# Kernel tuning notes

Hardware: AMD Instinct MI355X
Metric: run time of the kernel (lower is better)

Reference implementation:

```python
import jax, jax.numpy as jnp
import numpy as np

DIM = 512
NUM_HEADS = 8
HEAD_DIM = DIM // NUM_HEADS
SCALE = HEAD_DIM ** -0.5


def setup_inputs() -> dict:
    key = jax.random.key(0)
    k1, k2, k3, k4 = jax.random.split(key, 4)
    x = jax.random.normal(k1, (4, 2048, DIM), dtype=jnp.float32)
    W_qkv = jax.random.normal(k2, (DIM, 3 * DIM), dtype=jnp.float32) * (DIM ** -0.5)
    W_proj = jax.random.normal(k3, (DIM, DIM), dtype=jnp.float32) * (DIM ** -0.5)
    b_proj = jax.random.normal(k4, (DIM,), dtype=jnp.float32) * 0.01
    return {"x": x, "W_qkv": W_qkv, "W_proj": W_proj, "b_proj": b_proj}


def reference(x, W_qkv, W_proj, b_proj):
    B, N, C = x.shape
    H, hd = NUM_HEADS, HEAD_DIM
    # qkv: [B, N, 3, H, hd] -> (q, k, v) each [B, H, N, hd]
    qkv = (x @ W_qkv).reshape(B, N, 3, H, hd)
    qkv = jnp.transpose(qkv, (2, 0, 3, 1, 4))
    q, k, v = qkv[0], qkv[1], qkv[2]
    # eager attention: [B, H, N, N]
    attn = jnp.einsum('bhnd,bhmd->bhnm', q, k) * SCALE
    attn = jax.nn.softmax(attn, axis=-1)
    out = jnp.einsum('bhnm,bhmd->bhnd', attn, v)  # [B, H, N, hd]
    out = jnp.transpose(out, (0, 2, 1, 3)).reshape(B, N, C)
    out = out @ W_proj + b_proj
    return (out, k, v)
```

## Files before the change

kernel.cpp:

```cpp
#include <hip/hip_runtime.h>

typedef unsigned short ushort_t;
typedef __bf16 bf16x8 __attribute__((ext_vector_type(8)));
typedef __bf16 bf16x4 __attribute__((ext_vector_type(4)));
typedef ushort_t u16x8 __attribute__((ext_vector_type(8)));
typedef float f32x4 __attribute__((ext_vector_type(4)));

#define MFMA(a, b, c) __builtin_amdgcn_mfma_f32_16x16x32_bf16(a, b, c, 0, 0, 0)

#if __has_builtin(__builtin_amdgcn_mfma_f32_16x16x16bf16_1k)
typedef short s16x4 __attribute__((ext_vector_type(4)));
__device__ __forceinline__ f32x4 mfma16(bf16x4 a, bf16x4 b, f32x4 c) {
    union { bf16x4 v; s16x4 s; } ua, ub; ua.v = a; ub.v = b;
    return __builtin_amdgcn_mfma_f32_16x16x16bf16_1k(ua.s, ub.s, c, 0, 0, 0);
}
#define MFMA16_ASM 0
#elif __has_builtin(__builtin_amdgcn_mfma_f32_16x16x16_bf16)
__device__ __forceinline__ f32x4 mfma16(bf16x4 a, bf16x4 b, f32x4 c) {
    return __builtin_amdgcn_mfma_f32_16x16x16_bf16(a, b, c, 0, 0, 0);
}
#define MFMA16_ASM 0
#else
__device__ __forceinline__ f32x4 mfma16(bf16x4 a, bf16x4 b, f32x4 c) {
    asm("v_mfma_f32_16x16x16_bf16 %0, %1, %2, %0" : "+v"(c) : "v"(a), "v"(b));
    return c;
}
#define MFMA16_ASM 1
#endif

#define N_X      4194304L
#define N_WQKV   786432L
#define N_WPROJ  262144L
#define OUT_OFF_K 4194304L
#define OUT_OFF_V 8388608L

#define OFF_FLAG   0UL
#define OFF_XB     1024UL
#define OFF_WQKVT  (OFF_XB + 8388608UL)
#define OFF_WPROJT (OFF_WQKVT + 1572864UL)
#define OFF_BPROJ  (OFF_WPROJT + 524288UL)
#define OFF_QB     (OFF_BPROJ + 2048UL)
#define OFF_KB     (OFF_QB + 8388608UL)
#define OFF_VTB    (OFF_KB + 8388608UL)
#define OFF_ATTN   (OFF_VTB + 8388608UL)

#define QSCALE 0.180336880519191f

__device__ __forceinline__ ushort_t f2b(float f) {
    union { float f; unsigned u; } v; v.f = f;
    return (ushort_t)((v.u + 0x7FFFu + ((v.u >> 16) & 1u)) >> 16);
}
__device__ __forceinline__ ushort_t f2b_trunc(float f) {
    union { float f; unsigned u; } v; v.f = f;
    return (ushort_t)(v.u >> 16);
}
__device__ __forceinline__ float b2f(ushort_t h) {
    union { unsigned u; float f; } v; v.u = ((unsigned)h) << 16;
    return v.f;
}

__device__ __forceinline__ float fast_exp2(float x) {
#if __has_builtin(__builtin_amdgcn_exp2f)
    return __builtin_amdgcn_exp2f(x);
#else
    return __expf(x * 0.6931471805599453f);
#endif
}

__device__ __forceinline__ void glds16(const void* g, const void* l) {
    __builtin_amdgcn_global_load_lds((__attribute__((address_space(1))) void*)g,
                                     (__attribute__((address_space(3))) void*)l,
                                     16, 0, 0);
}

__device__ __forceinline__ int detect_bf16(const unsigned* __restrict__ x) {
    int lane = threadIdx.x & 63;
    int cnt = 0;
#pragma unroll
    for (int i = 0; i < 4; ++i) {
        unsigned w = x[lane + i * 64];
        float v = __uint_as_float((w & 0xFFFFu) << 16);
        float a = fabsf(v);
        if (a > 1e-3f && a < 100.0f) cnt++;
    }
#pragma unroll
    for (int off = 1; off < 64; off <<= 1) cnt += __shfl_xor(cnt, off, 64);
    return cnt > 128;
}

__global__ void k_prep(const void* __restrict__ xv, const void* __restrict__ wqv,
                       const void* __restrict__ wpv, const void* __restrict__ bpv,
                       ushort_t* __restrict__ xb, ushort_t* __restrict__ wqT,
                       ushort_t* __restrict__ wpT, float* __restrict__ bpf) {
    const int isb = detect_bf16((const unsigned*)xv);
    long i0 = (long)blockIdx.x * blockDim.x + threadIdx.x;
    long stride = (long)gridDim.x * blockDim.x;
    if (isb) {
        const ushort_t* x = (const ushort_t*)xv;
        const ushort_t* wq = (const ushort_t*)wqv;
        const ushort_t* wp = (const ushort_t*)wpv;
        const ushort_t* bp = (const ushort_t*)bpv;
        for (long i = i0; i < N_X / 8; i += stride)
            ((u16x8*)xb)[i] = ((const u16x8*)x)[i];
        for (long i = i0; i < N_WQKV / 8; i += stride) {
            long n = (i * 8) >> 9, k = (i * 8) & 511;
            u16x8 o;
#pragma unroll
            for (int e = 0; e < 8; ++e) o[e] = wq[(k + e) * 1536 + n];
            ((u16x8*)wqT)[i] = o;
        }
        for (long i = i0; i < N_WPROJ / 8; i += stride) {
            long n = (i * 8) >> 9, k = (i * 8) & 511;
            u16x8 o;
#pragma unroll
            for (int e = 0; e < 8; ++e) o[e] = wp[(k + e) * 512 + n];
            ((u16x8*)wpT)[i] = o;
        }
        for (long i = i0; i < 512; i += stride) bpf[i] = b2f(bp[i]);
    } else {
        const float* x = (const float*)xv;
        const float* wq = (const float*)wqv;
        const float* wp = (const float*)wpv;
        const float* bp = (const float*)bpv;
        for (long i = i0; i < N_X / 8; i += stride) {
            f32x4 a = ((const f32x4*)x)[i * 2], b = ((const f32x4*)x)[i * 2 + 1];
            u16x8 o;
#pragma unroll
            for (int e = 0; e < 4; ++e) { o[e] = f2b(a[e]); o[e + 4] = f2b(b[e]); }
            ((u16x8*)xb)[i] = o;
        }
        for (long i = i0; i < N_WQKV / 8; i += stride) {
            long n = (i * 8) >> 9, k = (i * 8) & 511;
            u16x8 o;
#pragma unroll
            for (int e = 0; e < 8; ++e) o[e] = f2b(wq[(k + e) * 1536 + n]);
            ((u16x8*)wqT)[i] = o;
        }
        for (long i = i0; i < N_WPROJ / 8; i += stride) {
            long n = (i * 8) >> 9, k = (i * 8) & 511;
            u16x8 o;
#pragma unroll
            for (int e = 0; e < 8; ++e) o[e] = f2b(wp[(k + e) * 512 + n]);
            ((u16x8*)wpT)[i] = o;
        }
        for (long i = i0; i < 512; i += stride) bpf[i] = bp[i];
    }
}

__global__ __launch_bounds__(256, 2)
void k_qkv(const unsigned* __restrict__ xraw,
           const ushort_t* __restrict__ xb, const ushort_t* __restrict__ wqT,
           ushort_t* __restrict__ qb, ushort_t* __restrict__ kb, ushort_t* __restrict__ vb,
           void* __restrict__ dout) {
    const int isb = detect_bf16(xraw);
    __shared__ __align__(16) ushort_t As[2][128 * 32];
    __shared__ __align__(16) ushort_t Bs[2][128 * 32];
    const int tid = threadIdx.x, wave = tid >> 6, lane = tid & 63;
    const int id = blockIdx.x;
    const int xcd = id & 7, g = id >> 3;
    const int bx = xcd * 8 + (g & 7);
    const int by = g >> 3;
    const int tm = bx * 128, tn = by * 128;
    const int wm = (wave >> 1) * 64, wn = (wave & 1) * 64;
    const int l15 = lane & 15, lq = lane >> 4;
    const int srow = lane >> 2, sc = lane & 3;

    f32x4 acc[4][4];
#pragma unroll
    for (int a = 0; a < 4; ++a)
#pragma unroll
        for (int b = 0; b < 4; ++b) acc[a][b] = (f32x4){0.f, 0.f, 0.f, 0.f};

    auto stage = [&](int k0, int buf) {
#pragma unroll
        for (int t = 0; t < 2; ++t) {
            int s = wave * 2 + t;
            int row = s * 16 + srow;
            int c = (sc ^ (row >> 1)) & 3;
            glds16(xb  + (long)(tm + row) * 512 + k0 + c * 8, &As[buf][s * 512]);
            glds16(wqT + (long)(tn + row) * 512 + k0 + c * 8, &Bs[buf][s * 512]);
        }
    };

    stage(0, 0);
    for (int ks = 0; ks < 16; ++ks) {
        int cur = ks & 1;
        if (ks < 15) {
            stage((ks + 1) * 32, cur ^ 1);
            asm volatile("s_waitcnt vmcnt(4)" ::: "memory");
        } else {
            asm volatile("s_waitcnt vmcnt(0)" ::: "memory");
        }
        __builtin_amdgcn_sched_barrier(0);
        __builtin_amdgcn_s_barrier();

        const ushort_t* Ac = &As[cur][0];
        const ushort_t* Bc = &Bs[cur][0];
        bf16x8 af[4], bfr[4];
#pragma unroll
        for (int mt = 0; mt < 4; ++mt) {
            int row = wm + mt * 16 + l15;
            int cp = (lq ^ (row >> 1)) & 3;
            af[mt] = *(const bf16x8*)(Ac + row * 32 + cp * 8);
        }
#pragma unroll
        for (int nt = 0; nt < 4; ++nt) {
            int row = wn + nt * 16 + l15;
            int cp = (lq ^ (row >> 1)) & 3;
            bfr[nt] = *(const bf16x8*)(Bc + row * 32 + cp * 8);
        }
#pragma unroll
        for (int mt = 0; mt < 4; ++mt)
#pragma unroll
            for (int nt = 0; nt < 4; ++nt)
                acc[mt][nt] = MFMA(af[mt], bfr[nt], acc[mt][nt]);

        asm volatile("s_waitcnt lgkmcnt(0)" ::: "memory");
        __builtin_amdgcn_sched_barrier(0);
        __builtin_amdgcn_s_barrier();
    }

    float*    koutf = (float*)dout + OUT_OFF_K;
    float*    voutf = (float*)dout + OUT_OFF_V;
    ushort_t* koutb = (ushort_t*)dout + OUT_OFF_K;
    ushort_t* voutb = (ushort_t*)dout + OUT_OFF_V;
#pragma unroll
    for (int mt = 0; mt < 4; ++mt) {
#pragma unroll
        for (int nt = 0; nt < 4; ++nt) {
            int j = tn + wn + nt * 16 + l15;
            int t = j >> 9, h = (j >> 6) & 7, d = j & 63;
#pragma unroll
            for (int r = 0; r < 4; ++r) {
                int mm = tm + wm + mt * 16 + lq * 4 + r;
                int b = mm >> 11, nn = mm & 2047;
                float v = acc[mt][nt][r];
                long idx = ((long)(b * 8 + h) * 2048 + nn) * 64 + d;
                if (t == 0) {
                    qb[idx] = f2b(v * QSCALE);
                } else if (t == 1) {
                    kb[idx] = f2b(v);
                    if (isb) koutb[idx] = f2b(v); else koutf[idx] = v;
                } else {
                    vb[idx] = f2b(v);
                    if (isb) voutb[idx] = f2b(v); else voutf[idx] = v;
                }
            }
        }
    }
}

__global__ __launch_bounds__(256, 4)
void k_vtrans(const ushort_t* __restrict__ vb, ushort_t* __restrict__ vtb) {
    __shared__ ushort_t T[64 * 64];
    const int tid = threadIdx.x;
    const int bh = blockIdx.y, ktile = blockIdx.x;
    const long base = (long)bh * 131072 + (long)ktile * 64 * 64;
    const int row = tid >> 2, cq = tid & 3;
#pragma unroll
    for (int half = 0; half < 2; ++half) {
        int c = cq + half * 4;
        u16x8 v = *(const u16x8*)(vb + base + row * 64 + c * 8);
#pragma unroll
        for (int e = 0; e < 8; ++e) {
            int dim = c * 8 + e;
            T[row * 64 + ((dim + row) & 63)] = v[e];
        }
    }
    __syncthreads();
#pragma unroll
    for (int it = 0; it < 16; ++it) {
        int d = (tid >> 6) * 16 + it;
        int key = tid & 63;
        vtb[(long)bh * 131072 + (long)d * 2048 + ktile * 64 + key] =
            T[key * 64 + ((d + key) & 63)];
    }
}

__global__ __launch_bounds__(256, 2)
void k_attn(const ushort_t* __restrict__ qb, const ushort_t* __restrict__ kb,
            const ushort_t* __restrict__ vtb, ushort_t* __restrict__ attnb) {
    __shared__ __align__(16) ushort_t Kt[2][128 * 64];
    __shared__ __align__(16) ushort_t Vt[2][64 * 128];
    const int tid = threadIdx.x, wave = tid >> 6, lane = tid & 63;
    const int l15 = lane & 15, lq = lane >> 4;
    const int id = blockIdx.x;
    const int xcd = id & 7, g = id >> 3;
    const int bh = xcd * 4 + (g >> 4);
    const int qt = g & 15;
    const long kvbase = (long)bh * 131072;
    const long qbase = kvbase + (long)qt * 128 * 64;

    const int ksrow = lane >> 3, kschunk = lane & 7;
    const int vsrow = lane >> 4, vschunk = lane & 15;

    auto stage = [&](int j, int buf) {
#pragma unroll
        for (int t = 0; t < 4; ++t) {
            int s = wave * 4 + t;
            {
                int row = s * 8 + ksrow;
                int c = kschunk ^ (row & 7);
                glds16(kb + kvbase + (long)(j * 128 + row) * 64 + c * 8, &Kt[buf][s * 512]);
            }
            {
                int row = s * 4 + vsrow;
                int c = vschunk ^ (row & 15);
                glds16(vtb + kvbase + (long)row * 2048 + j * 128 + c * 8, &Vt[buf][s * 512]);
            }
        }
    };

    stage(0, 0);

    bf16x8 aQ[2][2];
#pragma unroll
    for (int mq = 0; mq < 2; ++mq)
#pragma unroll
        for (int kt = 0; kt < 2; ++kt)
            aQ[mq][kt] = *(const bf16x8*)(qb + qbase +
                (long)(wave * 32 + mq * 16 + l15) * 64 + kt * 32 + lq * 8);

    f32x4 oacc[2][4];
#pragma unroll
    for (int mq = 0; mq < 2; ++mq)
#pragma unroll
        for (int nd = 0; nd < 4; ++nd) oacc[mq][nd] = (f32x4){0.f, 0.f, 0.f, 0.f};
    float ssum[2] = {0.f, 0.f};

    for (int j = 0; j < 16; ++j) {
        int cur = j & 1;
        if (j < 15) {
            stage(j + 1, cur ^ 1);
            asm volatile("s_waitcnt vmcnt(8)" ::: "memory");
        } else {
            asm volatile("s_waitcnt vmcnt(0)" ::: "memory");
        }
        __builtin_amdgcn_sched_barrier(0);
        __builtin_amdgcn_s_barrier();

        const ushort_t* Ktc = &Kt[cur][0];
        const ushort_t* Vtc = &Vt[cur][0];

#pragma unroll
        for (int h = 0; h < 2; ++h) {
            f32x4 sacc[2][4];
#pragma unroll
            for (int mq = 0; mq < 2; ++mq)
#pragma unroll
                for (int nt = 0; nt < 4; ++nt) sacc[mq][nt] = (f32x4){0.f, 0.f, 0.f, 0.f};
#pragma unroll
            for (int nt = 0; nt < 4; ++nt) {
                int krow = h * 64 + nt * 16 + l15;
#pragma unroll
                for (int kt = 0; kt < 2; ++kt) {
                    int c = (kt * 4 + lq) ^ (krow & 7);
                    bf16x8 bk = *(const bf16x8*)(Ktc + krow * 64 + c * 8);
                    sacc[0][nt] = MFMA(bk, aQ[0][kt], sacc[0][nt]);
                    sacc[1][nt] = MFMA(bk, aQ[1][kt], sacc[1][nt]);
                }
            }
            bf16x4 pb[2][4];
#pragma unroll
            for (int mq = 0; mq < 2; ++mq) {
#pragma unroll
                for (int nt = 0; nt < 4; ++nt) {
                    union { ushort_t u[4]; bf16x4 v; } pk;
                    float acc0 = 0.f, acc1 = 0.f;
#pragma unroll
                    for (int r = 0; r < 4; ++r) {
                        float p = fast_exp2(sacc[mq][nt][r]);
                        ushort_t tt = f2b_trunc(p);
                        pk.u[r] = tt;
                        if (r & 1) acc1 += b2f(tt); else acc0 += b2f(tt);
                    }
                    ssum[mq] += acc0 + acc1;
                    pb[mq][nt] = pk.v;
                }
            }
#pragma unroll
            for (int nd = 0; nd < 4; ++nd) {
                int drow = nd * 16 + l15;
#pragma unroll
                for (int nt = 0; nt < 4; ++nt) {
                    int kc = h * 8 + nt * 2 + (lq >> 1);
                    int cc = kc ^ (drow & 15);
                    bf16x4 va = *(const bf16x4*)(Vtc + drow * 128 + cc * 8 + (lq & 1) * 4);
                    oacc[0][nd] = mfma16(va, pb[0][nt], oacc[0][nd]);
                    oacc[1][nd] = mfma16(va, pb[1][nt], oacc[1][nd]);
                }
            }
        }

        asm volatile("s_waitcnt lgkmcnt(0)" ::: "memory");
        __builtin_amdgcn_sched_barrier(0);
        __builtin_amdgcn_s_barrier();
    }

#if MFMA16_ASM
    asm volatile("s_nop 7\n\ts_nop 7");
#endif
    const int b = bh >> 3, hh = bh & 7;
#pragma unroll
    for (int mq = 0; mq < 2; ++mq) {
        float s = ssum[mq];
        s += __shfl_xor(s, 16, 64);
        s += __shfl_xor(s, 32, 64);
        float inv = 1.0f / s;
        int n = qt * 128 + wave * 32 + mq * 16 + l15;
        long rowbase = ((long)b * 2048 + n) * 512 + hh * 64;
#pragma unroll
        for (int nd = 0; nd < 4; ++nd) {
            int d0 = nd * 16 + lq * 4;
            union { ushort_t u[4]; unsigned long long ll; } o;
#pragma unroll
            for (int r = 0; r < 4; ++r) o.u[r] = f2b(oacc[mq][nd][r] * inv);
            *(unsigned long long*)(attnb + rowbase + d0) = o.ll;
        }
    }
}

__global__ __launch_bounds__(256, 2)
void k_proj(const unsigned* __restrict__ xraw,
            const ushort_t* __restrict__ ab, const ushort_t* __restrict__ wpT,
            const float* __restrict__ bpf, void* __restrict__ dout) {
    const int isb = detect_bf16(xraw);
    __shared__ __align__(16) ushort_t As[2][128 * 32];
    __shared__ __align__(16) ushort_t Bs[2][128 * 32];
    const int tid = threadIdx.x, wave = tid >> 6, lane = tid & 63;
    const int id = blockIdx.x;
    const int xcd = id & 7, g = id >> 3;
    const int bx = xcd * 8 + (g & 7);
    const int by = g >> 3;
    const int tm = bx * 128, tn = by * 128;
    const int wm = (wave >> 1) * 64, wn = (wave & 1) * 64;
    const int l15 = lane & 15, lq = lane >> 4;
    const int srow = lane >> 2, sc = lane & 3;

    f32x4 acc[4][4];
#pragma unroll
    for (int a = 0; a < 4; ++a)
#pragma unroll
        for (int b = 0; b < 4; ++b) acc[a][b] = (f32x4){0.f, 0.f, 0.f, 0.f};

    auto stage = [&](int k0, int buf) {
#pragma unroll
        for (int t = 0; t < 2; ++t) {
            int s = wave * 2 + t;
            int row = s * 16 + srow;
            int c = (sc ^ (row >> 1)) & 3;
            glds16(ab  + (long)(tm + row) * 512 + k0 + c * 8, &As[buf][s * 512]);
            glds16(wpT + (long)(tn + row) * 512 + k0 + c * 8, &Bs[buf][s * 512]);
        }
    };

    stage(0, 0);
    for (int ks = 0; ks < 16; ++ks) {
        int cur = ks & 1;
        if (ks < 15) {
            stage((ks + 1) * 32, cur ^ 1);
            asm volatile("s_waitcnt vmcnt(4)" ::: "memory");
        } else {
            asm volatile("s_waitcnt vmcnt(0)" ::: "memory");
        }
        __builtin_amdgcn_sched_barrier(0);
        __builtin_amdgcn_s_barrier();

        const ushort_t* Ac = &As[cur][0];
        const ushort_t* Bc = &Bs[cur][0];
        bf16x8 af[4], bfr[4];
#pragma unroll
        for (int mt = 0; mt < 4; ++mt) {
            int row = wm + mt * 16 + l15;
            int cp = (lq ^ (row >> 1)) & 3;
            af[mt] = *(const bf16x8*)(Ac + row * 32 + cp * 8);
        }
#pragma unroll
        for (int nt = 0; nt < 4; ++nt) {
            int row = wn + nt * 16 + l15;
            int cp = (lq ^ (row >> 1)) & 3;
            bfr[nt] = *(const bf16x8*)(Bc + row * 32 + cp * 8);
        }
#pragma unroll
        for (int mt = 0; mt < 4; ++mt)
#pragma unroll
            for (int nt = 0; nt < 4; ++nt)
                acc[mt][nt] = MFMA(af[mt], bfr[nt], acc[mt][nt]);

        asm volatile("s_waitcnt lgkmcnt(0)" ::: "memory");
        __builtin_amdgcn_sched_barrier(0);
        __builtin_amdgcn_s_barrier();
    }

#pragma unroll
    for (int mt = 0; mt < 4; ++mt) {
#pragma unroll
        for (int nt = 0; nt < 4; ++nt) {
            int j = tn + wn + nt * 16 + l15;
            float bias = bpf[j];
#pragma unroll
            for (int r = 0; r < 4; ++r) {
                int mm = tm + wm + mt * 16 + lq * 4 + r;
                float v = acc[mt][nt][r] + bias;
                if (isb) ((ushort_t*)dout)[(long)mm * 512 + j] = f2b(v);
                else     ((float*)dout)[(long)mm * 512 + j] = v;
            }
        }
    }
}

extern "C" void kernel_launch(void* const* d_in, const int* in_sizes, int n_in,
                              void* d_out, int out_size, void* d_ws, size_t ws_size,
                              hipStream_t stream) {
    (void)in_sizes; (void)n_in; (void)out_size; (void)ws_size;
    char* ws = (char*)d_ws;
    ushort_t* xb  = (ushort_t*)(ws + OFF_XB);
    ushort_t* wqT = (ushort_t*)(ws + OFF_WQKVT);
    ushort_t* wpT = (ushort_t*)(ws + OFF_WPROJT);
    float*    bpf = (float*)(ws + OFF_BPROJ);
    ushort_t* qb  = (ushort_t*)(ws + OFF_QB);
    ushort_t* kb  = (ushort_t*)(ws + OFF_KB);
    ushort_t* vtb = (ushort_t*)(ws + OFF_VTB);
    ushort_t* ab  = (ushort_t*)(ws + OFF_ATTN);
    ushort_t* vb  = (ushort_t*)(ws + OFF_ATTN);

    k_prep<<<1024, 256, 0, stream>>>(d_in[0], d_in[1], d_in[2], d_in[3],
                                     xb, wqT, wpT, bpf);

    k_qkv<<<768, 256, 0, stream>>>((const unsigned*)d_in[0], xb, wqT,
                                   qb, kb, vb, d_out);

    k_vtrans<<<dim3(32, 32), 256, 0, stream>>>(vb, vtb);

    k_attn<<<512, 256, 0, stream>>>(qb, kb, vtb, ab);

    k_proj<<<256, 256, 0, stream>>>((const unsigned*)d_in[0], ab, wpT, bpf, d_out);
}
```

Baseline: 180.5 us.

## Use 16x16x32 MFMA for PV with MFMA row sums; single-buffer GEMMs

The attention kernel now computes all 128 keys of a tile at once and permutes K rows at staging, so the exponentiated scores pack directly into bf16x8 operands. This lets the P·V product use the wider 16x16x32 MFMA instead of 16x16x16. Row sums are now produced by an MFMA against a ones vector, replacing the scalar accumulation and cross-lane shuffles, and P is converted with a rounding cast instead of truncation. Separately, the QKV and projection GEMMs drop their LDS double-buffered pipeline for a single buffer with __syncthreads, which gives up load/compute overlap in exchange for less LDS and simpler code.

```diff
diff --git a/kernel.cpp b/kernel.cpp
--- a/kernel.cpp
+++ b/kernel.cpp
@@ -2,31 +2,10 @@
 
 typedef unsigned short ushort_t;
 typedef __bf16 bf16x8 __attribute__((ext_vector_type(8)));
-typedef __bf16 bf16x4 __attribute__((ext_vector_type(4)));
 typedef ushort_t u16x8 __attribute__((ext_vector_type(8)));
 typedef float f32x4 __attribute__((ext_vector_type(4)));
 
 #define MFMA(a, b, c) __builtin_amdgcn_mfma_f32_16x16x32_bf16(a, b, c, 0, 0, 0)
-
-#if __has_builtin(__builtin_amdgcn_mfma_f32_16x16x16bf16_1k)
-typedef short s16x4 __attribute__((ext_vector_type(4)));
-__device__ __forceinline__ f32x4 mfma16(bf16x4 a, bf16x4 b, f32x4 c) {
-    union { bf16x4 v; s16x4 s; } ua, ub; ua.v = a; ub.v = b;
-    return __builtin_amdgcn_mfma_f32_16x16x16bf16_1k(ua.s, ub.s, c, 0, 0, 0);
-}
-#define MFMA16_ASM 0
-#elif __has_builtin(__builtin_amdgcn_mfma_f32_16x16x16_bf16)
-__device__ __forceinline__ f32x4 mfma16(bf16x4 a, bf16x4 b, f32x4 c) {
-    return __builtin_amdgcn_mfma_f32_16x16x16_bf16(a, b, c, 0, 0, 0);
-}
-#define MFMA16_ASM 0
-#else
-__device__ __forceinline__ f32x4 mfma16(bf16x4 a, bf16x4 b, f32x4 c) {
-    asm("v_mfma_f32_16x16x16_bf16 %0, %1, %2, %0" : "+v"(c) : "v"(a), "v"(b));
-    return c;
-}
-#define MFMA16_ASM 1
-#endif
 
 #define N_X      4194304L
 #define N_WQKV   786432L
@@ -49,10 +28,6 @@
 __device__ __forceinline__ ushort_t f2b(float f) {
     union { float f; unsigned u; } v; v.f = f;
     return (ushort_t)((v.u + 0x7FFFu + ((v.u >> 16) & 1u)) >> 16);
-}
-__device__ __forceinline__ ushort_t f2b_trunc(float f) {
-    union { float f; unsigned u; } v; v.f = f;
-    return (ushort_t)(v.u >> 16);
 }
 __device__ __forceinline__ float b2f(ushort_t h) {
     union { unsigned u; float f; } v; v.u = ((unsigned)h) << 16;
@@ -153,8 +128,8 @@
            ushort_t* __restrict__ qb, ushort_t* __restrict__ kb, ushort_t* __restrict__ vb,
            void* __restrict__ dout) {
     const int isb = detect_bf16(xraw);
-    __shared__ __align__(16) ushort_t As[2][128 * 32];
-    __shared__ __align__(16) ushort_t Bs[2][128 * 32];
+    __shared__ __align__(16) ushort_t As[128 * 32];
+    __shared__ __align__(16) ushort_t Bs[128 * 32];
     const int tid = threadIdx.x, wave = tid >> 6, lane = tid & 63;
     const int id = blockIdx.x;
     const int xcd = id & 7, g = id >> 3;
@@ -171,53 +146,35 @@
 #pragma unroll
         for (int b = 0; b < 4; ++b) acc[a][b] = (f32x4){0.f, 0.f, 0.f, 0.f};
 
-    auto stage = [&](int k0, int buf) {
+    for (int k0 = 0; k0 < 512; k0 += 32) {
 #pragma unroll
         for (int t = 0; t < 2; ++t) {
             int s = wave * 2 + t;
             int row = s * 16 + srow;
             int c = (sc ^ (row >> 1)) & 3;
-            glds16(xb  + (long)(tm + row) * 512 + k0 + c * 8, &As[buf][s * 512]);
-            glds16(wqT + (long)(tn + row) * 512 + k0 + c * 8, &Bs[buf][s * 512]);
-        }
-    };
-
-    stage(0, 0);
-    for (int ks = 0; ks < 16; ++ks) {
-        int cur = ks & 1;
-        if (ks < 15) {
-            stage((ks + 1) * 32, cur ^ 1);
-            asm volatile("s_waitcnt vmcnt(4)" ::: "memory");
-        } else {
-            asm volatile("s_waitcnt vmcnt(0)" ::: "memory");
-        }
-        __builtin_amdgcn_sched_barrier(0);
-        __builtin_amdgcn_s_barrier();
-
-        const ushort_t* Ac = &As[cur][0];
-        const ushort_t* Bc = &Bs[cur][0];
+            glds16(xb  + (long)(tm + row) * 512 + k0 + c * 8, As + s * 512);
+            glds16(wqT + (long)(tn + row) * 512 + k0 + c * 8, Bs + s * 512);
+        }
+        __syncthreads();
         bf16x8 af[4], bfr[4];
 #pragma unroll
         for (int mt = 0; mt < 4; ++mt) {
             int row = wm + mt * 16 + l15;
             int cp = (lq ^ (row >> 1)) & 3;
-            af[mt] = *(const bf16x8*)(Ac + row * 32 + cp * 8);
+            af[mt] = *(const bf16x8*)(As + row * 32 + cp * 8);
         }
 #pragma unroll
         for (int nt = 0; nt < 4; ++nt) {
             int row = wn + nt * 16 + l15;
             int cp = (lq ^ (row >> 1)) & 3;
-            bfr[nt] = *(const bf16x8*)(Bc + row * 32 + cp * 8);
+            bfr[nt] = *(const bf16x8*)(Bs + row * 32 + cp * 8);
         }
 #pragma unroll
         for (int mt = 0; mt < 4; ++mt)
 #pragma unroll
             for (int nt = 0; nt < 4; ++nt)
                 acc[mt][nt] = MFMA(af[mt], bfr[nt], acc[mt][nt]);
-
-        asm volatile("s_waitcnt lgkmcnt(0)" ::: "memory");
-        __builtin_amdgcn_sched_barrier(0);
-        __builtin_amdgcn_s_barrier();
+        __syncthreads();
     }
 
     float*    koutf = (float*)dout + OUT_OFF_K;
@@ -299,9 +256,11 @@
         for (int t = 0; t < 4; ++t) {
             int s = wave * 4 + t;
             {
-                int row = s * 8 + ksrow;
-                int c = kschunk ^ (row & 7);
-                glds16(kb + kvbase + (long)(j * 128 + row) * 64 + c * 8, &Kt[buf][s * 512]);
+                int p = s * 8 + ksrow;
+                int pos = p & 15;
+                int akey = ((p >> 5) << 5) + ((pos >> 2) << 3) + (pos & 3) + ((p >> 4) & 1) * 4;
+                int c = kschunk ^ (p & 7);
+                glds16(kb + kvbase + (long)(j * 128 + akey) * 64 + c * 8, &Kt[buf][s * 512]);
             }
             {
                 int row = s * 4 + vsrow;
@@ -321,12 +280,18 @@
             aQ[mq][kt] = *(const bf16x8*)(qb + qbase +
                 (long)(wave * 32 + mq * 16 + l15) * 64 + kt * 32 + lq * 8);
 
-    f32x4 oacc[2][4];
-#pragma unroll
-    for (int mq = 0; mq < 2; ++mq)
+    union { ushort_t u[8]; bf16x8 v; } oneu;
+#pragma unroll
+    for (int i = 0; i < 8; ++i) oneu.u[i] = 0x3F80;
+    const bf16x8 ones8 = oneu.v;
+
+    f32x4 oacc[2][4], sum_acc[2];
+#pragma unroll
+    for (int mq = 0; mq < 2; ++mq) {
 #pragma unroll
         for (int nd = 0; nd < 4; ++nd) oacc[mq][nd] = (f32x4){0.f, 0.f, 0.f, 0.f};
-    float ssum[2] = {0.f, 0.f};
+        sum_acc[mq] = (f32x4){0.f, 0.f, 0.f, 0.f};
+    }
 
     for (int j = 0; j < 16; ++j) {
         int cur = j & 1;
@@ -342,53 +307,44 @@
         const ushort_t* Ktc = &Kt[cur][0];
         const ushort_t* Vtc = &Vt[cur][0];
 
-#pragma unroll
-        for (int h = 0; h < 2; ++h) {
-            f32x4 sacc[2][4];
-#pragma unroll
-            for (int mq = 0; mq < 2; ++mq)
-#pragma unroll
-                for (int nt = 0; nt < 4; ++nt) sacc[mq][nt] = (f32x4){0.f, 0.f, 0.f, 0.f};
-#pragma unroll
-            for (int nt = 0; nt < 4; ++nt) {
-                int krow = h * 64 + nt * 16 + l15;
-#pragma unroll
-                for (int kt = 0; kt < 2; ++kt) {
-                    int c = (kt * 4 + lq) ^ (krow & 7);
-                    bf16x8 bk = *(const bf16x8*)(Ktc + krow * 64 + c * 8);
-                    sacc[0][nt] = MFMA(bk, aQ[0][kt], sacc[0][nt]);
-                    sacc[1][nt] = MFMA(bk, aQ[1][kt], sacc[1][nt]);
-                }
-            }
-            bf16x4 pb[2][4];
-#pragma unroll
-            for (int mq = 0; mq < 2; ++mq) {
-#pragma unroll
-                for (int nt = 0; nt < 4; ++nt) {
-                    union { ushort_t u[4]; bf16x4 v; } pk;
-                    float acc0 = 0.f, acc1 = 0.f;
-#pragma unroll
-                    for (int r = 0; r < 4; ++r) {
-                        float p = fast_exp2(sacc[mq][nt][r]);
-                        ushort_t tt = f2b_trunc(p);
-                        pk.u[r] = tt;
-                        if (r & 1) acc1 += b2f(tt); else acc0 += b2f(tt);
-                    }
-                    ssum[mq] += acc0 + acc1;
-                    pb[mq][nt] = pk.v;
-                }
-            }
+        f32x4 sacc[2][8];
+#pragma unroll
+        for (int mq = 0; mq < 2; ++mq)
+#pragma unroll
+            for (int nt = 0; nt < 8; ++nt) sacc[mq][nt] = (f32x4){0.f, 0.f, 0.f, 0.f};
+#pragma unroll
+        for (int nt = 0; nt < 8; ++nt) {
+            int krow = nt * 16 + l15;
+#pragma unroll
+            for (int kt = 0; kt < 2; ++kt) {
+                int c = (kt * 4 + lq) ^ (krow & 7);
+                bf16x8 bk = *(const bf16x8*)(Ktc + krow * 64 + c * 8);
+                sacc[0][nt] = MFMA(bk, aQ[0][kt], sacc[0][nt]);
+                sacc[1][nt] = MFMA(bk, aQ[1][kt], sacc[1][nt]);
+            }
+        }
+
+        bf16x8 pb8[2][4];
+#pragma unroll
+        for (int mq = 0; mq < 2; ++mq)
+#pragma unroll
+            for (int nt = 0; nt < 8; ++nt)
+#pragma unroll
+                for (int r = 0; r < 4; ++r)
+                    pb8[mq][nt >> 1][(nt & 1) * 4 + r] =
+                        (__bf16)fast_exp2(sacc[mq][nt][r]);
+
+#pragma unroll
+        for (int t = 0; t < 4; ++t) {
+            sum_acc[0] = MFMA(ones8, pb8[0][t], sum_acc[0]);
+            sum_acc[1] = MFMA(ones8, pb8[1][t], sum_acc[1]);
 #pragma unroll
             for (int nd = 0; nd < 4; ++nd) {
                 int drow = nd * 16 + l15;
-#pragma unroll
-                for (int nt = 0; nt < 4; ++nt) {
-                    int kc = h * 8 + nt * 2 + (lq >> 1);
-                    int cc = kc ^ (drow & 15);
-                    bf16x4 va = *(const bf16x4*)(Vtc + drow * 128 + cc * 8 + (lq & 1) * 4);
-                    oacc[0][nd] = mfma16(va, pb[0][nt], oacc[0][nd]);
-                    oacc[1][nd] = mfma16(va, pb[1][nt], oacc[1][nd]);
-                }
+                int cc = (t * 4 + lq) ^ (drow & 15);
+                bf16x8 va = *(const bf16x8*)(Vtc + drow * 128 + cc * 8);
+                oacc[0][nd] = MFMA(va, pb8[0][t], oacc[0][nd]);
+                oacc[1][nd] = MFMA(va, pb8[1][t], oacc[1][nd]);
             }
         }
 
@@ -397,16 +353,10 @@
         __builtin_amdgcn_s_barrier();
     }
 
-#if MFMA16_ASM
-    asm volatile("s_nop 7\n\ts_nop 7");
-#endif
     const int b = bh >> 3, hh = bh & 7;
 #pragma unroll
     for (int mq = 0; mq < 2; ++mq) {
-        float s = ssum[mq];
-        s += __shfl_xor(s, 16, 64);
-        s += __shfl_xor(s, 32, 64);
-        float inv = 1.0f / s;
+        float inv = 1.0f / sum_acc[mq][0];
         int n = qt * 128 + wave * 32 + mq * 16 + l15;
         long rowbase = ((long)b * 2048 + n) * 512 + hh * 64;
 #pragma unroll
@@ -425,8 +375,8 @@
             const ushort_t* __restrict__ ab, const ushort_t* __restrict__ wpT,
             const float* __restrict__ bpf, void* __restrict__ dout) {
     const int isb = detect_bf16(xraw);
-    __shared__ __align__(16) ushort_t As[2][128 * 32];
-    __shared__ __align__(16) ushort_t Bs[2][128 * 32];
+    __shared__ __align__(16) ushort_t As[128 * 32];
+    __shared__ __align__(16) ushort_t Bs[128 * 32];
     const int tid = threadIdx.x, wave = tid >> 6, lane = tid & 63;
     const int id = blockIdx.x;
     const int xcd = id & 7, g = id >> 3;
@@ -443,53 +393,35 @@
 #pragma unroll
         for (int b = 0; b < 4; ++b) acc[a][b] = (f32x4){0.f, 0.f, 0.f, 0.f};
 
-    auto stage = [&](int k0, int buf) {
+    for (int k0 = 0; k0 < 512; k0 += 32) {
 #pragma unroll
         for (int t = 0; t < 2; ++t) {
             int s = wave * 2 + t;
             int row = s * 16 + srow;
             int c = (sc ^ (row >> 1)) & 3;
-            glds16(ab  + (long)(tm + row) * 512 + k0 + c * 8, &As[buf][s * 512]);
-            glds16(wpT + (long)(tn + row) * 512 + k0 + c * 8, &Bs[buf][s * 512]);
-        }
-    };
-
-    stage(0, 0);
-    for (int ks = 0; ks < 16; ++ks) {
-        int cur = ks & 1;
-        if (ks < 15) {
-            stage((ks + 1) * 32, cur ^ 1);
-            asm volatile("s_waitcnt vmcnt(4)" ::: "memory");
-        } else {
-            asm volatile("s_waitcnt vmcnt(0)" ::: "memory");
-        }
-        __builtin_amdgcn_sched_barrier(0);
-        __builtin_amdgcn_s_barrier();
-
-        const ushort_t* Ac = &As[cur][0];
-        const ushort_t* Bc = &Bs[cur][0];
+            glds16(ab  + (long)(tm + row) * 512 + k0 + c * 8, As + s * 512);
+            glds16(wpT + (long)(tn + row) * 512 + k0 + c * 8, Bs + s * 512);
+        }
+        __syncthreads();
         bf16x8 af[4], bfr[4];
 #pragma unroll
         for (int mt = 0; mt < 4; ++mt) {
             int row = wm + mt * 16 + l15;
             int cp = (lq ^ (row >> 1)) & 3;
-            af[mt] = *(const bf16x8*)(Ac + row * 32 + cp * 8);
+            af[mt] = *(const bf16x8*)(As + row * 32 + cp * 8);
         }
 #pragma unroll
         for (int nt = 0; nt < 4; ++nt) {
             int row = wn + nt * 16 + l15;
             int cp = (lq ^ (row >> 1)) & 3;
-            bfr[nt] = *(const bf16x8*)(Bc + row * 32 + cp * 8);
+            bfr[nt] = *(const bf16x8*)(Bs + row * 32 + cp * 8);
         }
 #pragma unroll
         for (int mt = 0; mt < 4; ++mt)
 #pragma unroll
             for (int nt = 0; nt < 4; ++nt)
                 acc[mt][nt] = MFMA(af[mt], bfr[nt], acc[mt][nt]);
-
-        asm volatile("s_waitcnt lgkmcnt(0)" ::: "memory");
-        __builtin_amdgcn_sched_barrier(0);
-        __builtin_amdgcn_s_barrier();
+        __syncthreads();
     }
 
 #pragma unroll
```

Result: faster. 167.2 us (-7.4%).
